# Kernel tuning notes

Measured on AMD Instinct MI355X. Metric: run time of the kernel, lower is better.

## Reference

```python
import jax, jax.numpy as jnp
import numpy as np

N_NODES = 20000
DIM = 512
N_EDGES = 320000  # first N_NODES edges are self-loops so every node has a predecessor
EPS = 1e-7


def _logmap0(y):
    # Poincare ball (c=1) log map at origin: artanh(||y||) * y / ||y||
    n = jnp.linalg.norm(y, axis=-1, keepdims=True)
    nc = jnp.clip(n, EPS, 1.0 - 1e-6)
    return jnp.arctanh(nc) * y / nc


def _expmap0(v):
    # Poincare ball (c=1) exp map at origin: tanh(||v||) * v / ||v||
    n = jnp.linalg.norm(v, axis=-1, keepdims=True)
    nc = jnp.maximum(n, EPS)
    return jnp.tanh(nc) * v / nc


def setup_inputs() -> dict:
    key = jax.random.key(0)
    ks = jax.random.split(key, 9)
    x_raw = jax.random.normal(ks[0], (N_NODES, DIM), dtype=jnp.float32)
    nrm = jnp.linalg.norm(x_raw, axis=-1, keepdims=True)
    x = 0.7 * x_raw / (1.0 + nrm)  # strictly inside the unit ball

    rng = np.random.RandomState(0)
    src_rand = rng.randint(0, N_NODES, size=N_EDGES - N_NODES)
    dst_rand = rng.randint(0, N_NODES, size=N_EDGES - N_NODES)
    loop = np.arange(N_NODES)
    src = jnp.asarray(np.concatenate([loop, src_rand]), dtype=jnp.int32)
    dst = jnp.asarray(np.concatenate([loop, dst_rand]), dtype=jnp.int32)

    s = 1.0 / np.sqrt(DIM)
    Wq = jax.random.normal(ks[1], (DIM, DIM), jnp.float32) * s
    bq = jax.random.normal(ks[2], (DIM,), jnp.float32) * 0.01
    Wk = jax.random.normal(ks[3], (DIM, DIM), jnp.float32) * s
    bk = jax.random.normal(ks[4], (DIM,), jnp.float32) * 0.01
    Wv = jax.random.normal(ks[5], (DIM, DIM), jnp.float32) * s
    bv = jax.random.normal(ks[6], (DIM,), jnp.float32) * 0.01
    Wo = jax.random.normal(ks[7], (DIM, DIM), jnp.float32) * s
    bo = jax.random.normal(ks[8], (DIM,), jnp.float32) * 0.01
    return dict(x=x, src=src, dst=dst, Wq=Wq, bq=bq, Wk=Wk, bk=bk,
                Wv=Wv, bv=bv, Wo=Wo, bo=bo)


def reference(x, src, dst, Wq, bq, Wk, bk, Wv, bv, Wo, bo):
    n_nodes, d = x.shape
    scale = 1.0 / jnp.sqrt(jnp.asarray(d, x.dtype))

    t = _logmap0(x)                                  # [N, d] tangent vectors
    q = (t @ Wq.T + bq) * scale                      # torch MHA scales q
    k = t @ Wk.T + bk
    v = t @ Wv.T + bv

    # Per-destination attention over predecessor (src) neighbors.
    scores = jnp.sum(q[dst] * k[src], axis=-1)       # [E]
    m = jax.ops.segment_max(scores, dst, num_segments=n_nodes)
    e = jnp.exp(scores - m[dst])
    denom = jax.ops.segment_sum(e, dst, num_segments=n_nodes)
    alpha = e / denom[dst]                           # [E] softmax weights

    attn = jax.ops.segment_sum(alpha[:, None] * v[src], dst,
                               num_segments=n_nodes)  # [N, d]
    new_h = attn @ Wo.T + bo                          # MHA output projection
    return _expmap0(new_h)
```

## Files before the change

### kernel.cpp

```cpp
#include <hip/hip_runtime.h>
#include <math.h>
#include <stdint.h>

#define NND 20000
#define DIMK 512
#define NE  320000

typedef __attribute__((ext_vector_type(8))) short short8;
typedef __attribute__((ext_vector_type(4))) float floatx4;
typedef __attribute__((ext_vector_type(2))) float float2v;

__device__ inline float bf2f(unsigned short h) {
    unsigned int u = ((unsigned int)h) << 16;
    return __uint_as_float(u);
}
__device__ inline unsigned short f2bf(float f) {
    unsigned int u = __float_as_uint(f);
    unsigned int r = (u + 0x7fffu + ((u >> 16) & 1u)) >> 16;
    return (unsigned short)r;
}

__device__ __forceinline__ void gld_lds16(const unsigned short* g, unsigned short* l) {
    __builtin_amdgcn_global_load_lds(
        (const __attribute__((address_space(1))) void*)g,
        (__attribute__((address_space(3))) void*)l,
        16, 0, 0);
}

__global__ __launch_bounds__(256) void k_pre(const float* __restrict__ x,
                                             const float* __restrict__ Wq,
                                             const float* __restrict__ Wk,
                                             const float* __restrict__ Wv,
                                             const float* __restrict__ Wo,
                                             const float* __restrict__ bq,
                                             const float* __restrict__ bk,
                                             const float* __restrict__ bv,
                                             const int* __restrict__ dst,
                                             int* __restrict__ counts,
                                             unsigned short* __restrict__ t,
                                             unsigned short* __restrict__ Wqkv,
                                             unsigned short* __restrict__ Wob,
                                             float* __restrict__ biasf,
                                             float scale_q) {
    int blk = blockIdx.x, tid = threadIdx.x;
    if (blk < 5000) {
        int row = blk * 4 + (tid >> 6);
        int lane = tid & 63;
        const floatx4* xp = (const floatx4*)(x + (size_t)row * DIMK + lane * 8);
        floatx4 x0 = xp[0], x1 = xp[1];
        float ss = 0.f;
#pragma unroll
        for (int i = 0; i < 4; i++) { ss += x0[i] * x0[i]; ss += x1[i] * x1[i]; }
#pragma unroll
        for (int off = 32; off >= 1; off >>= 1) ss += __shfl_xor(ss, off, 64);
        float n  = sqrtf(ss);
        float nc = fminf(fmaxf(n, 1e-7f), 1.0f - 1e-6f);
        float fac = atanhf(nc) / nc;
        union { short8 v; unsigned short u[8]; } o;
#pragma unroll
        for (int i = 0; i < 4; i++) { o.u[i] = f2bf(fac * x0[i]); o.u[4 + i] = f2bf(fac * x1[i]); }
        *(short8*)(t + (size_t)row * DIMK + lane * 8) = o.v;
    } else if (blk < 6024) {
        int i = (blk - 5000) * 256 + tid;
        int m = i >> 16, j = i & 65535;
        const float* in; unsigned short* out; float sc = 1.0f;
        if (m == 0)      { in = Wq; out = Wqkv;               sc = scale_q; }
        else if (m == 1) { in = Wk; out = Wqkv + 512 * DIMK;  sc = 16.0f; }
        else if (m == 2) { in = Wv; out = Wqkv + 1024 * DIMK; sc = 16.0f; }
        else             { in = Wo; out = Wob; }
        floatx4 f = *(const floatx4*)(in + (size_t)j * 4);
        union { unsigned long long d; unsigned short u[4]; } o;
#pragma unroll
        for (int q = 0; q < 4; q++) o.u[q] = f2bf(f[q] * sc);
        *(unsigned long long*)(out + (size_t)j * 4) = o.d;
    } else if (blk < 6030) {
        int i = (blk - 6024) * 256 + tid;
        if (i < 512) biasf[i] = bq[i] * scale_q;
        else if (i < 1024) biasf[i] = bk[i - 512] * 16.0f;
        else if (i < 1536) biasf[i] = bv[i - 1024] * 16.0f;
    } else {
        int e = (blk - 6030) * 256 + tid;
        if (e < NE) atomicAdd(&counts[dst[e]], 1);
    }
}

__global__ __launch_bounds__(256) void k_gemm(const unsigned short* __restrict__ A,
                                              const unsigned short* __restrict__ B,
                                              const float* __restrict__ biasf,
                                              unsigned short* __restrict__ out_q,
                                              unsigned char*  __restrict__ out_kv8,
                                              float* __restrict__ out_f,
                                              int M, int MT, int NT, int Ncols) {
    __shared__ unsigned short smem[16384];
    int b = blockIdx.x;
    int xcd = b & 7, i = b >> 3;
    int nt = i % NT, mt = (i / NT) * 8 + xcd;
    if (mt >= MT) return;
    int m0 = mt * 128, n0 = nt * 128;
    int tid = threadIdx.x, wv = tid >> 6, ln = tid & 63;
    int lr = ln & 15, qd = ln >> 4;
    int mh = wv >> 1, nh = wv & 1;

    floatx4 acc[4][4] = {};
    int srow = wv * 16 + (ln >> 2);
    int scol = (((ln & 3) ^ (ln >> 4)) & 3) * 8;
    int fsw = (qd ^ (lr >> 2)) & 3;

    {
        unsigned short* Ab = smem;
        unsigned short* Bb = smem + 8192;
#pragma unroll
        for (int p = 0; p < 2; p++) {
            int tr = p * 64 + srow;
            int ar = m0 + tr; if (ar > M - 1) ar = M - 1;
            gld_lds16(A + (size_t)ar * DIMK + scol, Ab + (p * 64 + wv * 16) * 32);
            gld_lds16(B + (size_t)(n0 + tr) * DIMK + scol, Bb + (p * 64 + wv * 16) * 32);
        }
    }

    for (int it = 0; it < 16; it++) {
        int cur = it & 1, nxt = cur ^ 1;
        __syncthreads();
        if (it + 1 < 16) {
            int kb = (it + 1) * 32;
            unsigned short* Ab = smem + nxt * 4096;
            unsigned short* Bb = smem + 8192 + nxt * 4096;
#pragma unroll
            for (int p = 0; p < 2; p++) {
                int tr = p * 64 + srow;
                int ar = m0 + tr; if (ar > M - 1) ar = M - 1;
                gld_lds16(A + (size_t)ar * DIMK + kb + scol, Ab + (p * 64 + wv * 16) * 32);
                gld_lds16(B + (size_t)(n0 + tr) * DIMK + kb + scol, Bb + (p * 64 + wv * 16) * 32);
            }
        }
        const unsigned short* Ac = smem + cur * 4096;
        const unsigned short* Bc = smem + 8192 + cur * 4096;
        short8 af[4], bfr[4];
#pragma unroll
        for (int mi = 0; mi < 4; mi++)
            af[mi] = *(const short8*)(Ac + (mh * 64 + mi * 16 + lr) * 32 + fsw * 8);
#pragma unroll
        for (int ni = 0; ni < 4; ni++)
            bfr[ni] = *(const short8*)(Bc + (nh * 64 + ni * 16 + lr) * 32 + fsw * 8);
#pragma unroll
        for (int mi = 0; mi < 4; mi++)
#pragma unroll
            for (int ni = 0; ni < 4; ni++)
                acc[mi][ni] = __builtin_amdgcn_mfma_f32_16x16x32_bf16(af[mi], bfr[ni], acc[mi][ni], 0, 0, 0);
    }

    float bb[4];
#pragma unroll
    for (int ni = 0; ni < 4; ni++) bb[ni] = biasf[n0 + nh * 64 + ni * 16 + lr];

    if (!out_f) {
        int region = nt >> 2;
        int col0 = (nt & 3) * 128;
        unsigned short* cs = smem;
#pragma unroll
        for (int g = 0; g < 4; g++) {
            __syncthreads();
            if (mh == (g >> 1)) {
                int miB = (g & 1) * 2;
#pragma unroll
                for (int m2 = 0; m2 < 2; m2++) {
                    int mi = miB + m2;
                    int lrow = mi * 16 + qd * 4 - (g & 1) * 32;
#pragma unroll
                    for (int ni = 0; ni < 4; ni++) {
                        int col = nh * 64 + ni * 16 + lr;
#pragma unroll
                        for (int r = 0; r < 4; r++)
                            cs[(lrow + r) * 128 + col] = f2bf(acc[mi][ni][r] + bb[ni]);
                    }
                }
            }
            __syncthreads();
#pragma unroll
            for (int itr = 0; itr < 2; itr++) {
                int slot = itr * 256 + tid;
                int row = slot >> 4, cg = slot & 15;
                int gm = m0 + g * 32 + row;
                if (gm < M) {
                    short8 vv = *(const short8*)(cs + row * 128 + cg * 8);
                    if (region == 0) {
                        *(short8*)(out_q + (size_t)gm * 512 + col0 + cg * 8) = vv;
                    } else {
                        union { short8 v; unsigned short u[8]; } pk; pk.v = vv;
                        int w0 = 0, w1 = 0;
                        w0 = __builtin_amdgcn_cvt_pk_fp8_f32(bf2f(pk.u[0]), bf2f(pk.u[1]), w0, false);
                        w0 = __builtin_amdgcn_cvt_pk_fp8_f32(bf2f(pk.u[2]), bf2f(pk.u[3]), w0, true);
                        w1 = __builtin_amdgcn_cvt_pk_fp8_f32(bf2f(pk.u[4]), bf2f(pk.u[5]), w1, false);
                        w1 = __builtin_amdgcn_cvt_pk_fp8_f32(bf2f(pk.u[6]), bf2f(pk.u[7]), w1, true);
                        uint2 o; o.x = (unsigned int)w0; o.y = (unsigned int)w1;
                        size_t off = (size_t)gm * 1024 + (region == 2 ? 512 : 0) + col0 + cg * 8;
                        *(uint2*)(out_kv8 + off) = o;
                    }
                }
            }
        }
    } else {
#pragma unroll
        for (int ni = 0; ni < 4; ni++) {
            int gn = n0 + nh * 64 + ni * 16 + lr;
#pragma unroll
            for (int mi = 0; mi < 4; mi++) {
                int gm0 = m0 + mh * 64 + mi * 16 + qd * 4;
#pragma unroll
                for (int r = 0; r < 4; r++) {
                    int gm = gm0 + r;
                    if (gm < M) out_f[(size_t)gm * Ncols + gn] = acc[mi][ni][r] + bb[ni];
                }
            }
        }
    }
}

__global__ __launch_bounds__(1024) void k_scan(const int* __restrict__ counts,
                                               int* __restrict__ offsets,
                                               int* __restrict__ pos) {
    const int C = 20;
    __shared__ int wsum[16];
    __shared__ int wpre[16];
    int tid = threadIdx.x, lane = tid & 63, w = tid >> 6;
    int local[C];
    int run = 0;
#pragma unroll
    for (int i = 0; i < C; i++) {
        int idx = tid * C + i;
        int c = (idx < NND) ? counts[idx] : 0;
        local[i] = run; run += c;
    }
    int v = run;
#pragma unroll
    for (int off = 1; off < 64; off <<= 1) {
        int u = __shfl_up(v, off, 64);
        if (lane >= off) v += u;
    }
    if (lane == 63) wsum[w] = v;
    __syncthreads();
    if (tid == 0) { int acc = 0; for (int i = 0; i < 16; i++) { wpre[i] = acc; acc += wsum[i]; } }
    __syncthreads();
    int texcl = wpre[w] + (v - run);
#pragma unroll
    for (int i = 0; i < C; i++) {
        int idx = tid * C + i;
        if (idx < NND) { int o = texcl + local[i]; offsets[idx] = o; pos[idx] = o; }
    }
    if (tid == 1023) offsets[NND] = texcl + run;
}

__global__ void k_scatter(const int* __restrict__ dst, const int* __restrict__ src,
                          int* __restrict__ pos, int* __restrict__ ssrc) {
    int e = blockIdx.x * 256 + threadIdx.x;
    if (e < NE) { int p = atomicAdd(&pos[dst[e]], 1); ssrc[p] = src[e]; }
}

__global__ __launch_bounds__(256) void k_fsa(const int* __restrict__ offsets,
                                             const int* __restrict__ ssrc,
                                             const unsigned short* __restrict__ qb,
                                             const unsigned char* __restrict__ kv8,
                                             unsigned short* __restrict__ attn) {
    __shared__ float sacc[4][512];
    __shared__ float sden[4];
    int n = blockIdx.x, tid = threadIdx.x, wv = tid >> 6, ln = tid & 63;
    int beg = offsets[n], end = offsets[n + 1];
    union { short8 v; unsigned short u[8]; } qu;
    qu.v = *(const short8*)(qb + (size_t)n * 512 + ln * 8);
    float2v qf2[4];
#pragma unroll
    for (int j = 0; j < 4; j++) {
        qf2[j].x = bf2f(qu.u[2 * j]);
        qf2[j].y = bf2f(qu.u[2 * j + 1]);
    }
    float2v av2[4] = {{0,0},{0,0},{0,0},{0,0}};
    float den = 0.f;
    int i = beg + wv * 2;
    for (; i + 1 < end; i += 8) {
        const unsigned char* p0 = kv8 + (size_t)ssrc[i] * 1024 + ln * 8;
        const unsigned char* p1 = kv8 + (size_t)ssrc[i + 1] * 1024 + ln * 8;
        uint2 kd0 = *(const uint2*)p0;
        uint2 kd1 = *(const uint2*)p1;
        float2v a0 = {0, 0}, a1 = {0, 0};
        float2v p;
        p = __builtin_amdgcn_cvt_pk_f32_fp8(kd0.x, false); a0 += qf2[0] * p;
        p = __builtin_amdgcn_cvt_pk_f32_fp8(kd0.x, true);  a0 += qf2[1] * p;
        p = __builtin_amdgcn_cvt_pk_f32_fp8(kd0.y, false); a0 += qf2[2] * p;
        p = __builtin_amdgcn_cvt_pk_f32_fp8(kd0.y, true);  a0 += qf2[3] * p;
        p = __builtin_amdgcn_cvt_pk_f32_fp8(kd1.x, false); a1 += qf2[0] * p;
        p = __builtin_amdgcn_cvt_pk_f32_fp8(kd1.x, true);  a1 += qf2[1] * p;
        p = __builtin_amdgcn_cvt_pk_f32_fp8(kd1.y, false); a1 += qf2[2] * p;
        p = __builtin_amdgcn_cvt_pk_f32_fp8(kd1.y, true);  a1 += qf2[3] * p;
        float d0 = a0.x + a0.y, d1 = a1.x + a1.y;
#pragma unroll
        for (int off = 32; off >= 1; off >>= 1) {
            d0 += __shfl_xor(d0, off, 64);
            d1 += __shfl_xor(d1, off, 64);
        }
        float w0 = __expf(d0), w1 = __expf(d1);
        den += w0 + w1;
        uint2 vd0 = *(const uint2*)(p0 + 512);
        uint2 vd1 = *(const uint2*)(p1 + 512);
        float2v w20 = {w0, w0}, w21 = {w1, w1};
        p = __builtin_amdgcn_cvt_pk_f32_fp8(vd0.x, false); av2[0] += w20 * p;
        p = __builtin_amdgcn_cvt_pk_f32_fp8(vd0.x, true);  av2[1] += w20 * p;
        p = __builtin_amdgcn_cvt_pk_f32_fp8(vd0.y, false); av2[2] += w20 * p;
        p = __builtin_amdgcn_cvt_pk_f32_fp8(vd0.y, true);  av2[3] += w20 * p;
        p = __builtin_amdgcn_cvt_pk_f32_fp8(vd1.x, false); av2[0] += w21 * p;
        p = __builtin_amdgcn_cvt_pk_f32_fp8(vd1.x, true);  av2[1] += w21 * p;
        p = __builtin_amdgcn_cvt_pk_f32_fp8(vd1.y, false); av2[2] += w21 * p;
        p = __builtin_amdgcn_cvt_pk_f32_fp8(vd1.y, true);  av2[3] += w21 * p;
    }
    if (i < end) {
        const unsigned char* p0 = kv8 + (size_t)ssrc[i] * 1024 + ln * 8;
        uint2 kd0 = *(const uint2*)p0;
        float2v a0 = {0, 0};
        float2v p;
        p = __builtin_amdgcn_cvt_pk_f32_fp8(kd0.x, false); a0 += qf2[0] * p;
        p = __builtin_amdgcn_cvt_pk_f32_fp8(kd0.x, true);  a0 += qf2[1] * p;
        p = __builtin_amdgcn_cvt_pk_f32_fp8(kd0.y, false); a0 += qf2[2] * p;
        p = __builtin_amdgcn_cvt_pk_f32_fp8(kd0.y, true);  a0 += qf2[3] * p;
        float d0 = a0.x + a0.y;
#pragma unroll
        for (int off = 32; off >= 1; off >>= 1) d0 += __shfl_xor(d0, off, 64);
        float w0 = __expf(d0);
        den += w0;
        uint2 vd0 = *(const uint2*)(p0 + 512);
        float2v w20 = {w0, w0};
        p = __builtin_amdgcn_cvt_pk_f32_fp8(vd0.x, false); av2[0] += w20 * p;
        p = __builtin_amdgcn_cvt_pk_f32_fp8(vd0.x, true);  av2[1] += w20 * p;
        p = __builtin_amdgcn_cvt_pk_f32_fp8(vd0.y, false); av2[2] += w20 * p;
        p = __builtin_amdgcn_cvt_pk_f32_fp8(vd0.y, true);  av2[3] += w20 * p;
    }
    floatx4 s0v = {av2[0].x, av2[0].y, av2[1].x, av2[1].y};
    floatx4 s1v = {av2[2].x, av2[2].y, av2[3].x, av2[3].y};
    *(floatx4*)&sacc[wv][ln * 8]     = s0v;
    *(floatx4*)&sacc[wv][ln * 8 + 4] = s1v;
    if (ln == 0) sden[wv] = den;
    __syncthreads();
    float inv = 0.0625f / (sden[0] + sden[1] + sden[2] + sden[3]);
    int c = tid * 2;
    float t0 = sacc[0][c] + sacc[1][c] + sacc[2][c] + sacc[3][c];
    float t1 = sacc[0][c + 1] + sacc[1][c + 1] + sacc[2][c + 1] + sacc[3][c + 1];
    attn[(size_t)n * 512 + c]     = f2bf(t0 * inv);
    attn[(size_t)n * 512 + c + 1] = f2bf(t1 * inv);
}

__global__ __launch_bounds__(64) void k_expmap(float* h) {
    int row = blockIdx.x, lane = threadIdx.x;
    floatx4* hp = (floatx4*)(h + (size_t)row * DIMK + lane * 8);
    floatx4 h0 = hp[0], h1 = hp[1];
    float ss = 0.f;
#pragma unroll
    for (int i = 0; i < 4; i++) { ss += h0[i] * h0[i]; ss += h1[i] * h1[i]; }
#pragma unroll
    for (int off = 32; off >= 1; off >>= 1) ss += __shfl_xor(ss, off, 64);
    float n  = sqrtf(ss);
    float nc = fmaxf(n, 1e-7f);
    float fac = tanhf(nc) / nc;
#pragma unroll
    for (int i = 0; i < 4; i++) { h0[i] *= fac; h1[i] *= fac; }
    hp[0] = h0; hp[1] = h1;
}

extern "C" void kernel_launch(void* const* d_in, const int* in_sizes, int n_in,
                              void* d_out, int out_size, void* d_ws, size_t ws_size,
                              hipStream_t stream) {
    const float* x  = (const float*)d_in[0];
    const int* src  = (const int*)d_in[1];
    const int* dst  = (const int*)d_in[2];
    const float* Wq = (const float*)d_in[3];
    const float* bq = (const float*)d_in[4];
    const float* Wk = (const float*)d_in[5];
    const float* bk = (const float*)d_in[6];
    const float* Wv = (const float*)d_in[7];
    const float* bv = (const float*)d_in[8];
    const float* Wo = (const float*)d_in[9];
    const float* bo = (const float*)d_in[10];
    float* out = (float*)d_out;

    char* ws = (char*)d_ws;
    const size_t RB = (size_t)NND * DIMK * 2;
    const size_t KVB = (size_t)NND * 1024;
    const size_t WB = (size_t)DIMK * DIMK * 2;
    unsigned short* t    = (unsigned short*)(ws);
    unsigned short* qb   = (unsigned short*)(ws + RB);
    unsigned char*  kv8  = (unsigned char*)(ws + 2 * RB);
    unsigned short* Wqkv = (unsigned short*)(ws + 2 * RB + KVB);
    unsigned short* Wob  = (unsigned short*)(ws + 2 * RB + KVB + 3 * WB);
    float* biasf         = (float*)(ws + 2 * RB + KVB + 4 * WB);
    char* p = ws + 2 * RB + KVB + 4 * WB + 1536 * 4;
    int* ssrc    = (int*)p;
    int* counts  = ssrc + NE;
    int* offsets = counts + NND;
    int* pos     = offsets + NND + 2;
    unsigned short* attn = t;

    hipMemsetAsync(counts, 0, (size_t)NND * 4, stream);

    const float scale_q = 0.04419417382415922f / 16.0f;
    k_pre<<<7280, 256, 0, stream>>>(x, Wq, Wk, Wv, Wo, bq, bk, bv, dst, counts,
                                    t, Wqkv, Wob, biasf, scale_q);

    k_scan<<<1, 1024, 0, stream>>>(counts, offsets, pos);
    k_scatter<<<(NE + 255) / 256, 256, 0, stream>>>(dst, src, pos, ssrc);

    k_gemm<<<8 * 20 * 12, 256, 0, stream>>>(t, Wqkv, biasf, qb, kv8, nullptr,
                                            NND, 157, 12, 1536);

    k_fsa<<<NND, 256, 0, stream>>>(offsets, ssrc, qb, kv8, attn);

    k_gemm<<<8 * 20 * 4, 256, 0, stream>>>(attn, Wob, bo, nullptr, nullptr, out,
                                           NND, 157, 4, 512);
    k_expmap<<<NND, 64, 0, stream>>>(out);
}
```

Baseline: 287.9 us.

## Fold K/V projections into query and output weights via precomputed weight products

Rewrites the attention algebra so that scores use q·(Wk^T) against the raw tangent vectors t, and values aggregate raw t and are projected later by the combined Wo·Wv matrix. The bk term is dropped because it is constant per destination and cancels in the softmax, and bv is folded into the output bias. The QKV GEMM shrinks from 1536 to 512 output columns and the FP8 K/V buffer is removed. In exchange the gather now reads 1 KB of bf16 per edge instead of 1 KB of fp8 K+V, and two small 512x512 weight-product GEMMs are added inside the scatter launch.

```diff
diff --git a/kernel.cpp b/kernel.cpp
--- a/kernel.cpp
+++ b/kernel.cpp
@@ -8,7 +8,6 @@
 
 typedef __attribute__((ext_vector_type(8))) short short8;
 typedef __attribute__((ext_vector_type(4))) float floatx4;
-typedef __attribute__((ext_vector_type(2))) float float2v;
 
 __device__ inline float bf2f(unsigned short h) {
     unsigned int u = ((unsigned int)h) << 16;
@@ -33,15 +32,18 @@
                                              const float* __restrict__ Wv,
                                              const float* __restrict__ Wo,
                                              const float* __restrict__ bq,
-                                             const float* __restrict__ bk,
                                              const float* __restrict__ bv,
+                                             const float* __restrict__ bo,
                                              const int* __restrict__ dst,
                                              int* __restrict__ counts,
                                              unsigned short* __restrict__ t,
-                                             unsigned short* __restrict__ Wqkv,
-                                             unsigned short* __restrict__ Wob,
-                                             float* __restrict__ biasf,
-                                             float scale_q) {
+                                             unsigned short* __restrict__ WqTs,
+                                             unsigned short* __restrict__ WkT,
+                                             unsigned short* __restrict__ WvT,
+                                             unsigned short* __restrict__ WoB,
+                                             float* __restrict__ bh,
+                                             float* __restrict__ bpr,
+                                             float scf) {
     int blk = blockIdx.x, tid = threadIdx.x;
     if (blk < 5000) {
         int row = blk * 4 + (tid >> 6);
@@ -60,26 +62,52 @@
 #pragma unroll
         for (int i = 0; i < 4; i++) { o.u[i] = f2bf(fac * x0[i]); o.u[4 + i] = f2bf(fac * x1[i]); }
         *(short8*)(t + (size_t)row * DIMK + lane * 8) = o.v;
-    } else if (blk < 6024) {
+    } else if (blk < 5256) {
         int i = (blk - 5000) * 256 + tid;
-        int m = i >> 16, j = i & 65535;
-        const float* in; unsigned short* out; float sc = 1.0f;
-        if (m == 0)      { in = Wq; out = Wqkv;               sc = scale_q; }
-        else if (m == 1) { in = Wk; out = Wqkv + 512 * DIMK;  sc = 16.0f; }
-        else if (m == 2) { in = Wv; out = Wqkv + 1024 * DIMK; sc = 16.0f; }
-        else             { in = Wo; out = Wob; }
-        floatx4 f = *(const floatx4*)(in + (size_t)j * 4);
+        floatx4 f = *(const floatx4*)(Wo + (size_t)i * 4);
         union { unsigned long long d; unsigned short u[4]; } o;
 #pragma unroll
-        for (int q = 0; q < 4; q++) o.u[q] = f2bf(f[q] * sc);
-        *(unsigned long long*)(out + (size_t)j * 4) = o.d;
-    } else if (blk < 6030) {
-        int i = (blk - 6024) * 256 + tid;
-        if (i < 512) biasf[i] = bq[i] * scale_q;
-        else if (i < 1024) biasf[i] = bk[i - 512] * 16.0f;
-        else if (i < 1536) biasf[i] = bv[i - 1024] * 16.0f;
+        for (int q = 0; q < 4; q++) o.u[q] = f2bf(f[q]);
+        *(unsigned long long*)(WoB + (size_t)i * 4) = o.d;
+    } else if (blk < 5448) {
+        int g = blk - 5256;
+        int m = g >> 6, tile = g & 63;
+        int tr = tile >> 3, tc = tile & 7;
+        const float* srcm = (m == 0) ? Wq : (m == 1) ? Wk : Wv;
+        unsigned short* dstp = (m == 0) ? WqTs : (m == 1) ? WkT : WvT;
+        float sc = (m == 0) ? scf : 1.0f;
+        __shared__ float tl[64][65];
+#pragma unroll
+        for (int i = 0; i < 16; i++) {
+            int idx = i * 256 + tid; int r = idx >> 6, c = idx & 63;
+            tl[c][r] = srcm[(size_t)(tr * 64 + r) * 512 + tc * 64 + c];
+        }
+        __syncthreads();
+#pragma unroll
+        for (int i = 0; i < 16; i++) {
+            int idx = i * 256 + tid; int r = idx >> 6, c = idx & 63;
+            dstp[(size_t)(tc * 64 + r) * 512 + tr * 64 + c] = f2bf(tl[r][c] * sc);
+        }
+    } else if (blk < 5450) {
+        int col = (blk - 5448) * 256 + tid;
+        float s = 0.f;
+#pragma unroll 8
+        for (int m = 0; m < 512; m++) s += bq[m] * Wk[(size_t)m * 512 + col];
+        bh[col] = s * scf;
+    } else if (blk < 5578) {
+        int row = (blk - 5450) * 4 + (tid >> 6);
+        int lane = tid & 63;
+        const floatx4* wp = (const floatx4*)(Wo + (size_t)row * 512 + lane * 8);
+        const floatx4* bp = (const floatx4*)(bv + lane * 8);
+        floatx4 a0 = wp[0], a1 = wp[1], c0 = bp[0], c1 = bp[1];
+        float s = 0.f;
+#pragma unroll
+        for (int i = 0; i < 4; i++) { s += a0[i] * c0[i]; s += a1[i] * c1[i]; }
+#pragma unroll
+        for (int off = 32; off >= 1; off >>= 1) s += __shfl_xor(s, off, 64);
+        if (lane == 0) bpr[row] = s + bo[row];
     } else {
-        int e = (blk - 6030) * 256 + tid;
+        int e = (blk - 5578) * 256 + tid;
         if (e < NE) atomicAdd(&counts[dst[e]], 1);
     }
 }
@@ -88,7 +116,6 @@
                                               const unsigned short* __restrict__ B,
                                               const float* __restrict__ biasf,
                                               unsigned short* __restrict__ out_q,
-                                              unsigned char*  __restrict__ out_kv8,
                                               float* __restrict__ out_f,
                                               int M, int MT, int NT, int Ncols) {
     __shared__ unsigned short smem[16384];
@@ -154,8 +181,7 @@
     for (int ni = 0; ni < 4; ni++) bb[ni] = biasf[n0 + nh * 64 + ni * 16 + lr];
 
     if (!out_f) {
-        int region = nt >> 2;
-        int col0 = (nt & 3) * 128;
+        int col0 = nt * 128;
         unsigned short* cs = smem;
 #pragma unroll
         for (int g = 0; g < 4; g++) {
@@ -183,19 +209,7 @@
                 int gm = m0 + g * 32 + row;
                 if (gm < M) {
                     short8 vv = *(const short8*)(cs + row * 128 + cg * 8);
-                    if (region == 0) {
-                        *(short8*)(out_q + (size_t)gm * 512 + col0 + cg * 8) = vv;
-                    } else {
-                        union { short8 v; unsigned short u[8]; } pk; pk.v = vv;
-                        int w0 = 0, w1 = 0;
-                        w0 = __builtin_amdgcn_cvt_pk_fp8_f32(bf2f(pk.u[0]), bf2f(pk.u[1]), w0, false);
-                        w0 = __builtin_amdgcn_cvt_pk_fp8_f32(bf2f(pk.u[2]), bf2f(pk.u[3]), w0, true);
-                        w1 = __builtin_amdgcn_cvt_pk_fp8_f32(bf2f(pk.u[4]), bf2f(pk.u[5]), w1, false);
-                        w1 = __builtin_amdgcn_cvt_pk_fp8_f32(bf2f(pk.u[6]), bf2f(pk.u[7]), w1, true);
-                        uint2 o; o.x = (unsigned int)w0; o.y = (unsigned int)w1;
-                        size_t off = (size_t)gm * 1024 + (region == 2 ? 512 : 0) + col0 + cg * 8;
-                        *(uint2*)(out_kv8 + off) = o;
-                    }
+                    *(short8*)(out_q + (size_t)gm * 512 + col0 + cg * 8) = vv;
                 }
             }
         }
@@ -250,16 +264,93 @@
     if (tid == 1023) offsets[NND] = texcl + run;
 }
 
-__global__ void k_scatter(const int* __restrict__ dst, const int* __restrict__ src,
-                          int* __restrict__ pos, int* __restrict__ ssrc) {
-    int e = blockIdx.x * 256 + threadIdx.x;
-    if (e < NE) { int p = atomicAdd(&pos[dst[e]], 1); ssrc[p] = src[e]; }
+__global__ __launch_bounds__(256) void k_scatter(const int* __restrict__ dst,
+                                                 const int* __restrict__ src,
+                                                 int* __restrict__ pos,
+                                                 int* __restrict__ ssrc,
+                                                 const unsigned short* __restrict__ WkT,
+                                                 const unsigned short* __restrict__ WqTs,
+                                                 const unsigned short* __restrict__ WoB,
+                                                 const unsigned short* __restrict__ WvT,
+                                                 unsigned short* __restrict__ Amat,
+                                                 unsigned short* __restrict__ Wovb) {
+    __shared__ unsigned short smem[16384];
+    int b = blockIdx.x;
+    if (b < 1250) {
+        int e = b * 256 + threadIdx.x;
+        if (e < NE) { int p = atomicAdd(&pos[dst[e]], 1); ssrc[p] = src[e]; }
+        return;
+    }
+    int g = b - 1250;
+    int prod = g >> 4;
+    int mt = (g >> 2) & 3, nt = g & 3;
+    const unsigned short* A = prod ? WoB : WkT;
+    const unsigned short* B = prod ? WvT : WqTs;
+    unsigned short* outp = prod ? Wovb : Amat;
+    int m0 = mt * 128, n0 = nt * 128;
+    int tid = threadIdx.x, wv = tid >> 6, ln = tid & 63;
+    int lr = ln & 15, qd = ln >> 4;
+    int mh = wv >> 1, nh = wv & 1;
+    floatx4 acc[4][4] = {};
+    int srow = wv * 16 + (ln >> 2);
+    int scol = (((ln & 3) ^ (ln >> 4)) & 3) * 8;
+    int fsw = (qd ^ (lr >> 2)) & 3;
+    {
+        unsigned short* Ab = smem;
+        unsigned short* Bb = smem + 8192;
+#pragma unroll
+        for (int p = 0; p < 2; p++) {
+            int tr = p * 64 + srow;
+            gld_lds16(A + (size_t)(m0 + tr) * DIMK + scol, Ab + (p * 64 + wv * 16) * 32);
+            gld_lds16(B + (size_t)(n0 + tr) * DIMK + scol, Bb + (p * 64 + wv * 16) * 32);
+        }
+    }
+    for (int it = 0; it < 16; it++) {
+        int cur = it & 1, nxt = cur ^ 1;
+        __syncthreads();
+        if (it + 1 < 16) {
+            int kb = (it + 1) * 32;
+            unsigned short* Ab = smem + nxt * 4096;
+            unsigned short* Bb = smem + 8192 + nxt * 4096;
+#pragma unroll
+            for (int p = 0; p < 2; p++) {
+                int tr = p * 64 + srow;
+                gld_lds16(A + (size_t)(m0 + tr) * DIMK + kb + scol, Ab + (p * 64 + wv * 16) * 32);
+                gld_lds16(B + (size_t)(n0 + tr) * DIMK + kb + scol, Bb + (p * 64 + wv * 16) * 32);
+            }
+        }
+        const unsigned short* Ac = smem + cur * 4096;
+        const unsigned short* Bc = smem + 8192 + cur * 4096;
+        short8 af[4], bfr[4];
+#pragma unroll
+        for (int mi = 0; mi < 4; mi++)
+            af[mi] = *(const short8*)(Ac + (mh * 64 + mi * 16 + lr) * 32 + fsw * 8);
+#pragma unroll
+        for (int ni = 0; ni < 4; ni++)
+            bfr[ni] = *(const short8*)(Bc + (nh * 64 + ni * 16 + lr) * 32 + fsw * 8);
+#pragma unroll
+        for (int mi = 0; mi < 4; mi++)
+#pragma unroll
+            for (int ni = 0; ni < 4; ni++)
+                acc[mi][ni] = __builtin_amdgcn_mfma_f32_16x16x32_bf16(af[mi], bfr[ni], acc[mi][ni], 0, 0, 0);
+    }
+#pragma unroll
+    for (int ni = 0; ni < 4; ni++) {
+        int gn = n0 + nh * 64 + ni * 16 + lr;
+#pragma unroll
+        for (int mi = 0; mi < 4; mi++) {
+            int gm0 = m0 + mh * 64 + mi * 16 + qd * 4;
+#pragma unroll
+            for (int r = 0; r < 4; r++)
+                outp[(size_t)(gm0 + r) * 512 + gn] = f2bf(acc[mi][ni][r]);
+        }
+    }
 }
 
 __global__ __launch_bounds__(256) void k_fsa(const int* __restrict__ offsets,
                                              const int* __restrict__ ssrc,
                                              const unsigned short* __restrict__ qb,
-                                             const unsigned char* __restrict__ kv8,
+                                             const unsigned short* __restrict__ tb,
                                              unsigned short* __restrict__ attn) {
     __shared__ float sacc[4][512];
     __shared__ float sden[4];
@@ -267,31 +358,25 @@
     int beg = offsets[n], end = offsets[n + 1];
     union { short8 v; unsigned short u[8]; } qu;
     qu.v = *(const short8*)(qb + (size_t)n * 512 + ln * 8);
-    float2v qf2[4];
-#pragma unroll
-    for (int j = 0; j < 4; j++) {
-        qf2[j].x = bf2f(qu.u[2 * j]);
-        qf2[j].y = bf2f(qu.u[2 * j + 1]);
-    }
-    float2v av2[4] = {{0,0},{0,0},{0,0},{0,0}};
+    float qf[8];
+#pragma unroll
+    for (int j = 0; j < 8; j++) qf[j] = bf2f(qu.u[j]);
+    float av[8] = {0, 0, 0, 0, 0, 0, 0, 0};
     float den = 0.f;
     int i = beg + wv * 2;
     for (; i + 1 < end; i += 8) {
-        const unsigned char* p0 = kv8 + (size_t)ssrc[i] * 1024 + ln * 8;
-        const unsigned char* p1 = kv8 + (size_t)ssrc[i + 1] * 1024 + ln * 8;
-        uint2 kd0 = *(const uint2*)p0;
-        uint2 kd1 = *(const uint2*)p1;
-        float2v a0 = {0, 0}, a1 = {0, 0};
-        float2v p;
-        p = __builtin_amdgcn_cvt_pk_f32_fp8(kd0.x, false); a0 += qf2[0] * p;
-        p = __builtin_amdgcn_cvt_pk_f32_fp8(kd0.x, true);  a0 += qf2[1] * p;
-        p = __builtin_amdgcn_cvt_pk_f32_fp8(kd0.y, false); a0 += qf2[2] * p;
-        p = __builtin_amdgcn_cvt_pk_f32_fp8(kd0.y, true);  a0 += qf2[3] * p;
-        p = __builtin_amdgcn_cvt_pk_f32_fp8(kd1.x, false); a1 += qf2[0] * p;
-        p = __builtin_amdgcn_cvt_pk_f32_fp8(kd1.x, true);  a1 += qf2[1] * p;
-        p = __builtin_amdgcn_cvt_pk_f32_fp8(kd1.y, false); a1 += qf2[2] * p;
-        p = __builtin_amdgcn_cvt_pk_f32_fp8(kd1.y, true);  a1 += qf2[3] * p;
-        float d0 = a0.x + a0.y, d1 = a1.x + a1.y;
+        const unsigned short* p0 = tb + (size_t)ssrc[i] * 512 + ln * 8;
+        const unsigned short* p1 = tb + (size_t)ssrc[i + 1] * 512 + ln * 8;
+        union { short8 v; unsigned short u[8]; } r0, r1;
+        r0.v = *(const short8*)p0;
+        r1.v = *(const short8*)p1;
+        float t0[8], t1[8];
+        float d0 = 0.f, d1 = 0.f;
+#pragma unroll
+        for (int j = 0; j < 8; j++) {
+            t0[j] = bf2f(r0.u[j]); d0 += qf[j] * t0[j];
+            t1[j] = bf2f(r1.u[j]); d1 += qf[j] * t1[j];
+        }
 #pragma unroll
         for (int off = 32; off >= 1; off >>= 1) {
             d0 += __shfl_xor(d0, off, 64);
@@ -299,46 +384,31 @@
         }
         float w0 = __expf(d0), w1 = __expf(d1);
         den += w0 + w1;
-        uint2 vd0 = *(const uint2*)(p0 + 512);
-        uint2 vd1 = *(const uint2*)(p1 + 512);
-        float2v w20 = {w0, w0}, w21 = {w1, w1};
-        p = __builtin_amdgcn_cvt_pk_f32_fp8(vd0.x, false); av2[0] += w20 * p;
-        p = __builtin_amdgcn_cvt_pk_f32_fp8(vd0.x, true);  av2[1] += w20 * p;
-        p = __builtin_amdgcn_cvt_pk_f32_fp8(vd0.y, false); av2[2] += w20 * p;
-        p = __builtin_amdgcn_cvt_pk_f32_fp8(vd0.y, true);  av2[3] += w20 * p;
-        p = __builtin_amdgcn_cvt_pk_f32_fp8(vd1.x, false); av2[0] += w21 * p;
-        p = __builtin_amdgcn_cvt_pk_f32_fp8(vd1.x, true);  av2[1] += w21 * p;
-        p = __builtin_amdgcn_cvt_pk_f32_fp8(vd1.y, false); av2[2] += w21 * p;
-        p = __builtin_amdgcn_cvt_pk_f32_fp8(vd1.y, true);  av2[3] += w21 * p;
+#pragma unroll
+        for (int j = 0; j < 8; j++) av[j] += w0 * t0[j] + w1 * t1[j];
     }
     if (i < end) {
-        const unsigned char* p0 = kv8 + (size_t)ssrc[i] * 1024 + ln * 8;
-        uint2 kd0 = *(const uint2*)p0;
-        float2v a0 = {0, 0};
-        float2v p;
-        p = __builtin_amdgcn_cvt_pk_f32_fp8(kd0.x, false); a0 += qf2[0] * p;
-        p = __builtin_amdgcn_cvt_pk_f32_fp8(kd0.x, true);  a0 += qf2[1] * p;
-        p = __builtin_amdgcn_cvt_pk_f32_fp8(kd0.y, false); a0 += qf2[2] * p;
-        p = __builtin_amdgcn_cvt_pk_f32_fp8(kd0.y, true);  a0 += qf2[3] * p;
-        float d0 = a0.x + a0.y;
+        const unsigned short* p0 = tb + (size_t)ssrc[i] * 512 + ln * 8;
+        union { short8 v; unsigned short u[8]; } r0;
+        r0.v = *(const short8*)p0;
+        float t0[8];
+        float d0 = 0.f;
+#pragma unroll
+        for (int j = 0; j < 8; j++) { t0[j] = bf2f(r0.u[j]); d0 += qf[j] * t0[j]; }
 #pragma unroll
         for (int off = 32; off >= 1; off >>= 1) d0 += __shfl_xor(d0, off, 64);
         float w0 = __expf(d0);
         den += w0;
-        uint2 vd0 = *(const uint2*)(p0 + 512);
-        float2v w20 = {w0, w0};
-        p = __builtin_amdgcn_cvt_pk_f32_fp8(vd0.x, false); av2[0] += w20 * p;
-        p = __builtin_amdgcn_cvt_pk_f32_fp8(vd0.x, true);  av2[1] += w20 * p;
-        p = __builtin_amdgcn_cvt_pk_f32_fp8(vd0.y, false); av2[2] += w20 * p;
-        p = __builtin_amdgcn_cvt_pk_f32_fp8(vd0.y, true);  av2[3] += w20 * p;
-    }
-    floatx4 s0v = {av2[0].x, av2[0].y, av2[1].x, av2[1].y};
-    floatx4 s1v = {av2[2].x, av2[2].y, av2[3].x, av2[3].y};
+#pragma unroll
+        for (int j = 0; j < 8; j++) av[j] += w0 * t0[j];
+    }
+    floatx4 s0v = {av[0], av[1], av[2], av[3]};
+    floatx4 s1v = {av[4], av[5], av[6], av[7]};
     *(floatx4*)&sacc[wv][ln * 8]     = s0v;
     *(floatx4*)&sacc[wv][ln * 8 + 4] = s1v;
     if (ln == 0) sden[wv] = den;
     __syncthreads();
-    float inv = 0.0625f / (sden[0] + sden[1] + sden[2] + sden[3]);
+    float inv = 1.0f / (sden[0] + sden[1] + sden[2] + sden[3]);
     int c = tid * 2;
     float t0 = sacc[0][c] + sacc[1][c] + sacc[2][c] + sacc[3][c];
     float t1 = sacc[0][c + 1] + sacc[1][c + 1] + sacc[2][c + 1] + sacc[3][c + 1];
@@ -372,7 +442,6 @@
     const float* Wq = (const float*)d_in[3];
     const float* bq = (const float*)d_in[4];
     const float* Wk = (const float*)d_in[5];
-    const float* bk = (const float*)d_in[6];
     const float* Wv = (const float*)d_in[7];
     const float* bv = (const float*)d_in[8];
     const float* Wo = (const float*)d_in[9];
@@ -380,37 +449,41 @@
     float* out = (float*)d_out;
 
     char* ws = (char*)d_ws;
-    const size_t RB = (size_t)NND * DIMK * 2;
-    const size_t KVB = (size_t)NND * 1024;
-    const size_t WB = (size_t)DIMK * DIMK * 2;
+    const size_t RB  = (size_t)NND * DIMK * 2;
+    const size_t WB  = (size_t)DIMK * DIMK * 2;
     unsigned short* t    = (unsigned short*)(ws);
-    unsigned short* qb   = (unsigned short*)(ws + RB);
-    unsigned char*  kv8  = (unsigned char*)(ws + 2 * RB);
-    unsigned short* Wqkv = (unsigned short*)(ws + 2 * RB + KVB);
-    unsigned short* Wob  = (unsigned short*)(ws + 2 * RB + KVB + 3 * WB);
-    float* biasf         = (float*)(ws + 2 * RB + KVB + 4 * WB);
-    char* p = ws + 2 * RB + KVB + 4 * WB + 1536 * 4;
+    unsigned short* qh   = (unsigned short*)(ws + RB);
+    unsigned short* WqTs = (unsigned short*)(ws + 2 * RB);
+    unsigned short* WkT  = (unsigned short*)(ws + 2 * RB + WB);
+    unsigned short* WvT  = (unsigned short*)(ws + 2 * RB + 2 * WB);
+    unsigned short* WoB  = (unsigned short*)(ws + 2 * RB + 3 * WB);
+    unsigned short* Amat = (unsigned short*)(ws + 2 * RB + 4 * WB);
+    unsigned short* Wovb = (unsigned short*)(ws + 2 * RB + 5 * WB);
+    float* bh            = (float*)(ws + 2 * RB + 6 * WB);
+    float* bpr           = (float*)(ws + 2 * RB + 6 * WB + 2048);
+    char* p = ws + 2 * RB + 6 * WB + 4096;
     int* ssrc    = (int*)p;
     int* counts  = ssrc + NE;
     int* offsets = counts + NND;
     int* pos     = offsets + NND + 2;
-    unsigned short* attn = t;
+    unsigned short* attn = qh;
 
     hipMemsetAsync(counts, 0, (size_t)NND * 4, stream);
 
-    const float scale_q = 0.04419417382415922f / 16.0f;
-    k_pre<<<7280, 256, 0, stream>>>(x, Wq, Wk, Wv, Wo, bq, bk, bv, dst, counts,
-                                    t, Wqkv, Wob, biasf, scale_q);
+    const float scf = 0.04419417382415922f;
+    k_pre<<<6828, 256, 0, stream>>>(x, Wq, Wk, Wv, Wo, bq, bv, bo, dst, counts,
+                                    t, WqTs, WkT, WvT, WoB, bh, bpr, scf);
 
     k_scan<<<1, 1024, 0, stream>>>(counts, offsets, pos);
-    k_scatter<<<(NE + 255) / 256, 256, 0, stream>>>(dst, src, pos, ssrc);
-
-    k_gemm<<<8 * 20 * 12, 256, 0, stream>>>(t, Wqkv, biasf, qb, kv8, nullptr,
-                                            NND, 157, 12, 1536);
-
-    k_fsa<<<NND, 256, 0, stream>>>(offsets, ssrc, qb, kv8, attn);
-
-    k_gemm<<<8 * 20 * 4, 256, 0, stream>>>(attn, Wob, bo, nullptr, nullptr, out,
+    k_scatter<<<1282, 256, 0, stream>>>(dst, src, pos, ssrc,
+                                        WkT, WqTs, WoB, WvT, Amat, Wovb);
+
+    k_gemm<<<8 * 20 * 4, 256, 0, stream>>>(t, Amat, bh, qh, nullptr,
+                                           NND, 157, 4, 512);
+
+    k_fsa<<<NND, 256, 0, stream>>>(offsets, ssrc, qh, t, attn);
+
+    k_gemm<<<8 * 20 * 4, 256, 0, stream>>>(attn, Wovb, bpr, nullptr, out,
                                            NND, 157, 4, 512);
     k_expmap<<<NND, 64, 0, stream>>>(out);
 }
```

Result: no change. 285.1 us (-1.0%).
